# Kernel tuning notes

Hardware: AMD Instinct MI355X
Metric: run time of the kernel (lower is better)

Reference implementation:

```python
import jax, jax.numpy as jnp
import numpy as np

MATRIC_TYPE = 0   # 0: corr, 1: cov
WEIGHT_IN = 1.0
WEIGHT_BET = 1.0


def setup_inputs() -> dict:
    key = jax.random.key(0)
    k1, k2, k3 = jax.random.split(key, 3)
    x = jax.random.normal(k1, (256, 128, 768), dtype=jnp.float32)
    label = jax.random.randint(k2, (256,), 0, 1000, dtype=jnp.int64 if jax.config.read('jax_enable_x64') else jnp.int32)
    genre_label = jax.random.randint(k3, (256,), 0, 8, dtype=jnp.int64 if jax.config.read('jax_enable_x64') else jnp.int32)
    return {"x": x, "label": label, "genre_label": genre_label}


def _compute_various(x):
    # x: [B, N, D] -> within (D,D), between (D,D)
    B, N, D = x.shape
    tol_num = B * N
    x_mean = jnp.mean(x, axis=1)                       # (B, D)
    mean = jnp.mean(x.reshape(-1, D), axis=0)          # (D,)
    res_x = x - x_mean[:, None, :]                     # (B, N, D)
    # fused batched scatter accumulation (replaces python loop of small mms)
    within = jnp.einsum('bnd,bne->de', res_x, res_x) / tol_num
    res_mean = x_mean - mean                           # (B, D)
    between = (N * (res_mean.T @ res_mean)) / tol_num
    return within, between


def _corr_normalize(m):
    # torch code: Diag=(d,1); mm(Diag.T, Diag)=(1,1) scalar = sum(diag^2)
    d = jnp.diagonal(m)
    s = jnp.sqrt(jnp.sum(d * d))
    return m / s


def reference(x, label, genre_label):
    input_x = x[::2]
    input_u = x[1::2]
    x1_within, x1_between = _compute_various(input_x)
    x2_within, x2_between = _compute_various(input_u)
    if MATRIC_TYPE == 0:
        x1_within = _corr_normalize(x1_within)
        x2_within = _corr_normalize(x2_within)
        x1_between = _corr_normalize(x1_between)
        x2_between = _corr_normalize(x2_between)
    within = jnp.sum((x1_within - x2_within) ** 2)
    between = jnp.sum((x1_between - x2_between) ** 2)
    return WEIGHT_IN * within + WEIGHT_BET * between
```

## Files before the change

kernel.cpp:

```cpp
#include <hip/hip_runtime.h>


typedef float f32x2 __attribute__((ext_vector_type(2)));
typedef float f32x4 __attribute__((ext_vector_type(4)));
typedef short bf16x8 __attribute__((ext_vector_type(8)));
typedef unsigned short u16x4 __attribute__((ext_vector_type(4)));

static constexpr size_t OFF_RT    = 0;
static constexpr size_t OFF_XM    = 50331648;
static constexpr size_t OFF_M     = 51118080;
static constexpr size_t OFF_RM    = 51124224;
static constexpr size_t OFF_P2    = 51517440;
static constexpr size_t OFF_BPART = 54269952;
static constexpr size_t OFF_P1    = 54355968;

__device__ __forceinline__ unsigned int f2bf_u32(float f) {
  union { float f; unsigned int u; } v; v.f = f;
  unsigned int u = v.u;
  unsigned int lsb = (u >> 16) & 1u;
  u += 0x7fffu + lsb;
  return u >> 16;
}

__device__ __forceinline__ void gload_lds16(const void* g, void* l) {
  __builtin_amdgcn_global_load_lds(
      (const __attribute__((address_space(1))) unsigned int*)g,
      (__attribute__((address_space(3))) unsigned int*)l, 16, 0, 0);
}

__global__ void __launch_bounds__(256) k1_means_convert(const float* __restrict__ x,
                                                        float* __restrict__ xm,
                                                        unsigned short* __restrict__ RT) {
  __shared__ unsigned short T[128][130];
  __shared__ float pm[4][128];
  int bid = blockIdx.x;
  int dt = bid % 6, borig = bid / 6;
  int s = borig & 1, b = borig >> 1;
  int tid = threadIdx.x, w = tid >> 6, lane = tid & 63;

  const float* xb = x + (size_t)borig * (128 * 768) + dt * 128 + 2 * lane;
  float cs0 = 0.f, cs1 = 0.f;
#pragma unroll
  for (int g = 0; g < 8; ++g) {
    int n0 = w * 32 + g * 4;
    f32x2 a0 = *reinterpret_cast<const f32x2*>(xb + (size_t)(n0 + 0) * 768);
    f32x2 a1 = *reinterpret_cast<const f32x2*>(xb + (size_t)(n0 + 1) * 768);
    f32x2 a2 = *reinterpret_cast<const f32x2*>(xb + (size_t)(n0 + 2) * 768);
    f32x2 a3 = *reinterpret_cast<const f32x2*>(xb + (size_t)(n0 + 3) * 768);
    cs0 += a0[0] + a1[0] + a2[0] + a3[0];
    cs1 += a0[1] + a1[1] + a2[1] + a3[1];
    u16x4 p0, p1;
    p0[0] = (unsigned short)f2bf_u32(a0[0]); p0[1] = (unsigned short)f2bf_u32(a1[0]);
    p0[2] = (unsigned short)f2bf_u32(a2[0]); p0[3] = (unsigned short)f2bf_u32(a3[0]);
    p1[0] = (unsigned short)f2bf_u32(a0[1]); p1[1] = (unsigned short)f2bf_u32(a1[1]);
    p1[2] = (unsigned short)f2bf_u32(a2[1]); p1[3] = (unsigned short)f2bf_u32(a3[1]);
    *reinterpret_cast<u16x4*>(&T[2 * lane + 0][n0]) = p0;
    *reinterpret_cast<u16x4*>(&T[2 * lane + 1][n0]) = p1;
  }
  *reinterpret_cast<f32x2*>(&pm[w][2 * lane]) = f32x2{cs0, cs1};
  __syncthreads();

  if (tid < 128) {
    float mv = (pm[0][tid] + pm[1][tid] + pm[2][tid] + pm[3][tid]) * (1.f / 128.f);
    xm[((size_t)(s * 128 + b)) * 768ull + dt * 128 + tid] = mv;
  }

  int half = lane >> 5;
  int nb = (lane & 31) * 4;
  unsigned short* rtbase = RT + (size_t)s * (768ull * 16384ull) + (size_t)(b * 128 + nb);
#pragma unroll
  for (int i = 0; i < 16; ++i) {
    int d_loc = w * 32 + 2 * i + half;
    uint2 v = *reinterpret_cast<const uint2*>(&T[d_loc][nb]);
    *reinterpret_cast<uint2*>(rtbase + (size_t)(dt * 128 + d_loc) * 16384ull) = v;
  }
}

__global__ void __launch_bounds__(256) k2_slice_mean(const float* __restrict__ xm,
                                                     float* __restrict__ m,
                                                     unsigned short* __restrict__ rmT) {
  __shared__ float pm[4][64];
  __shared__ float ml[64];
  int s = blockIdx.x / 12, dg = blockIdx.x % 12;
  int t = threadIdx.x;
  int d_loc = t & 63, part = t >> 6;
  int d = dg * 64 + d_loc;
  const float* base = xm + (size_t)s * 128ull * 768ull + d;
  float acc = 0.f;
#pragma unroll 4
  for (int i = 0; i < 32; ++i) acc += base[(size_t)(part * 32 + i) * 768ull];
  pm[part][d_loc] = acc;
  __syncthreads();
  if (t < 64) {
    float mv = (pm[0][t] + pm[1][t] + pm[2][t] + pm[3][t]) * (1.f / 128.f);
    m[s * 768 + dg * 64 + t] = mv;
    ml[t] = mv;
  }
  __syncthreads();
  float mv = ml[d_loc];
  unsigned short* rt = rmT + ((size_t)s * 768ull + d) * 128ull + part * 32;
#pragma unroll 4
  for (int i = 0; i < 32; ++i)
    rt[i] = (unsigned short)f2bf_u32(base[(size_t)(part * 32 + i) * 768ull] - mv);
}

__device__ __forceinline__ void stage_tile(const unsigned short* __restrict__ g, int KP, int k0,
                                           unsigned short* lds, int wave, int lane) {
#pragma unroll
  for (int i = 0; i < 4; ++i) {
    int cb = (i * 4 + wave) * 64;
    int chunk = cb + lane;
    int r = chunk >> 3, sl = chunk & 7;
    int ss = sl ^ (r & 7);
    const unsigned short* src = g + (size_t)r * KP + (k0 + ss * 8);
    gload_lds16(src, lds + (size_t)cb * 8);
  }
}

__device__ __forceinline__ bf16x8 read_frag(const unsigned short* lds, int row, int slot) {
  int chunk = row * 8 + (slot ^ (row & 7));
  return *reinterpret_cast<const bf16x8*>(lds + chunk * 8);
}

__device__ __forceinline__ void tp2tile(int tp, int& td, int& te) {
  td = 0; int t2 = tp;
  while (t2 >= 6 - td) { t2 -= 6 - td; ++td; }
  te = td + t2;
}

__global__ void __launch_bounds__(256) gemm_ata(const unsigned short* __restrict__ Rbig,
                                                const unsigned short* __restrict__ rmT,
                                                float* __restrict__ P1, float* __restrict__ P2,
                                                int ksplit) {
  __shared__ unsigned short Ta[2][128 * 64];
  __shared__ unsigned short Tb[2][128 * 64];
  int bid = blockIdx.x;
  const unsigned short* R; size_t slice_stride; int KP;
  int rest, step0, step1; float* pout;
  if (bid < 42 * ksplit) {
    R = Rbig; slice_stride = 768ull * 16384ull; KP = 16384;
    int c = bid % ksplit; rest = bid / ksplit;
    step0 = (256 * c) / ksplit; step1 = (256 * (c + 1)) / ksplit;
    pout = P1 + (size_t)bid * (128 * 128);
  } else {
    int b2 = bid - 42 * ksplit;
    R = rmT; slice_stride = 768ull * 128ull; KP = 128;
    rest = b2; step0 = 0; step1 = 2;
    pout = P2 + (size_t)b2 * (128 * 128);
  }
  int s = rest & 1; int tp = rest >> 1;
  int td, te; tp2tile(tp, td, te);
  bool diag = (td == te);
  const unsigned short* Ra = R + (size_t)s * slice_stride + (size_t)(td * 128) * KP;
  const unsigned short* Rb = R + (size_t)s * slice_stride + (size_t)(te * 128) * KP;
  int tid = threadIdx.x, wave = tid >> 6, lane = tid & 63;
  int m_off = (wave >> 1) * 64, n_off = (wave & 1) * 64;
  int row_a = m_off + (lane & 15), row_b = n_off + (lane & 15);
  f32x4 acc[4][4];
#pragma unroll
  for (int i = 0; i < 4; ++i)
#pragma unroll
    for (int j = 0; j < 4; ++j) { acc[i][j][0]=0.f; acc[i][j][1]=0.f; acc[i][j][2]=0.f; acc[i][j][3]=0.f; }

  stage_tile(Ra, KP, step0 * 64, Ta[0], wave, lane);
  if (!diag) stage_tile(Rb, KP, step0 * 64, Tb[0], wave, lane);
  __syncthreads();

  int cur = 0;
  for (int kt = step0; kt < step1; ++kt) {
    if (kt + 1 < step1) {
      stage_tile(Ra, KP, (kt + 1) * 64, Ta[cur ^ 1], wave, lane);
      if (!diag) stage_tile(Rb, KP, (kt + 1) * 64, Tb[cur ^ 1], wave, lane);
    }
    const unsigned short* Bsrc = diag ? Ta[cur] : Tb[cur];
#pragma unroll
    for (int ks = 0; ks < 2; ++ks) {
      bf16x8 a[4], b[4];
      int slot = ks * 4 + (lane >> 4);
#pragma unroll
      for (int mi = 0; mi < 4; ++mi) a[mi] = read_frag(Ta[cur], row_a + mi * 16, slot);
#pragma unroll
      for (int ni = 0; ni < 4; ++ni) b[ni] = read_frag(Bsrc, row_b + ni * 16, slot);
#pragma unroll
      for (int mi = 0; mi < 4; ++mi)
#pragma unroll
        for (int ni = 0; ni < 4; ++ni)
          acc[mi][ni] = __builtin_amdgcn_mfma_f32_16x16x32_bf16(a[mi], b[ni], acc[mi][ni], 0, 0, 0);
    }
    __syncthreads();
    cur ^= 1;
  }
  int hi = lane >> 4, lo = lane & 15;
#pragma unroll
  for (int mi = 0; mi < 4; ++mi)
#pragma unroll
    for (int ni = 0; ni < 4; ++ni)
#pragma unroll
      for (int r = 0; r < 4; ++r) {
        int rr = m_off + mi * 16 + hi * 4 + r;
        int cc = n_off + ni * 16 + lo;
        pout[rr * 128 + cc] = acc[mi][ni][r];
      }
}

__global__ void __launch_bounds__(256) k5_elem(const float* __restrict__ P1,
                                               const float* __restrict__ P2,
                                               const float* __restrict__ m,
                                               float* __restrict__ bpart, int ksplit) {
  __shared__ float red[4][10];
  int bid = blockIdx.x;
  int tp = bid >> 6;
  int td, te; tp2tile(tp, td, te);
  int idx = ((bid & 63) << 8) + threadIdx.x;
  int r = idx >> 7, cc = idx & 127;
  int d = td * 128 + r, e = te * 128 + cc;
  float W[2], B[2];
  for (int s = 0; s < 2; ++s) {
    const float* base1 = P1 + (size_t)((tp * 2 + s) * ksplit) * 16384ull + idx;
    float g1 = 0.f;
    for (int c6 = 0; c6 < ksplit; ++c6) g1 += base1[(size_t)c6 * 16384ull];
    float p2v = P2[(size_t)(tp * 2 + s) * 16384ull + idx];
    W[s] = g1 - 128.0f * p2v - 16384.0f * m[s * 768 + d] * m[s * 768 + e];
    B[s] = p2v;
  }
  float mult = (td != te) ? 2.0f : 1.0f;
  bool isdiag = (td == te) && (r == cc);
  float v[10];
  v[0] = W[0] * W[0] * mult;  v[1] = W[1] * W[1] * mult;  v[2] = W[0] * W[1] * mult;
  v[3] = B[0] * B[0] * mult;  v[4] = B[1] * B[1] * mult;  v[5] = B[0] * B[1] * mult;
  v[6] = isdiag ? W[0] * W[0] : 0.f;
  v[7] = isdiag ? W[1] * W[1] : 0.f;
  v[8] = isdiag ? B[0] * B[0] : 0.f;
  v[9] = isdiag ? B[1] * B[1] : 0.f;
  int lane = threadIdx.x & 63, w = threadIdx.x >> 6;
#pragma unroll
  for (int off = 32; off; off >>= 1)
#pragma unroll
    for (int j = 0; j < 10; ++j) v[j] += __shfl_down(v[j], off, 64);
  if (lane == 0)
#pragma unroll
    for (int j = 0; j < 10; ++j) red[w][j] = v[j];
  __syncthreads();
  if (threadIdx.x < 10) {
    int j = threadIdx.x;
    bpart[bid * 16 + j] = red[0][j] + red[1][j] + red[2][j] + red[3][j];
  }
}

__global__ void __launch_bounds__(256) k6_final(const float* __restrict__ bpart,
                                                float* __restrict__ out) {
  __shared__ float red[4][10];
  float acc[10];
#pragma unroll
  for (int j = 0; j < 10; ++j) acc[j] = 0.f;
  for (int i = threadIdx.x; i < 1344; i += 256)
#pragma unroll
    for (int j = 0; j < 10; ++j) acc[j] += bpart[i * 16 + j];
  int lane = threadIdx.x & 63, w = threadIdx.x >> 6;
#pragma unroll
  for (int off = 32; off; off >>= 1)
#pragma unroll
    for (int j = 0; j < 10; ++j) acc[j] += __shfl_down(acc[j], off, 64);
  if (lane == 0)
#pragma unroll
    for (int j = 0; j < 10; ++j) red[w][j] = acc[j];
  __syncthreads();
  if (threadIdx.x == 0) {
    float S[10];
#pragma unroll
    for (int j = 0; j < 10; ++j) S[j] = red[0][j] + red[1][j] + red[2][j] + red[3][j];
    float lw = S[0] / S[6] + S[1] / S[7] - 2.0f * S[2] / sqrtf(S[6] * S[7]);
    float lb = S[3] / S[8] + S[4] / S[9] - 2.0f * S[5] / sqrtf(S[8] * S[9]);
    out[0] = lw + lb;
  }
}

extern "C" void kernel_launch(void* const* d_in, const int* in_sizes, int n_in,
                              void* d_out, int out_size, void* d_ws, size_t ws_size,
                              hipStream_t stream) {
  const float* x = (const float*)d_in[0];
  char* ws = (char*)d_ws;
  unsigned short* RT  = (unsigned short*)(ws + OFF_RT);
  float* xm           = (float*)(ws + OFF_XM);
  float* m            = (float*)(ws + OFF_M);
  unsigned short* rmT = (unsigned short*)(ws + OFF_RM);
  float* P2           = (float*)(ws + OFF_P2);
  float* bpart        = (float*)(ws + OFF_BPART);
  float* P1           = (float*)(ws + OFF_P1);
  float* out          = (float*)d_out;

  size_t availP1 = (ws_size > OFF_P1) ? (ws_size - OFF_P1) : 0;
  int ksplit = (int)(availP1 / (42ull * 128 * 128 * 4));
  if (ksplit > 12) ksplit = 12;
  if (ksplit < 1) ksplit = 1;

  hipLaunchKernelGGL(k1_means_convert, dim3(1536), dim3(256), 0, stream, x, xm, RT);
  hipLaunchKernelGGL(k2_slice_mean, dim3(24), dim3(256), 0, stream, xm, m, rmT);
  hipLaunchKernelGGL(gemm_ata, dim3(42 * ksplit + 42), dim3(256), 0, stream,
                     RT, rmT, P1, P2, ksplit);
  hipLaunchKernelGGL(k5_elem, dim3(1344), dim3(256), 0, stream, P1, P2, m, bpart, ksplit);
  hipLaunchKernelGGL(k6_final, dim3(1), dim3(256), 0, stream, bpart, out);
}
```

Baseline: 77.75 us.

## Fuse final reduction into elementwise kernel via last-block atomic counter

Merges the elementwise partial-reduction kernel and the single-block final kernel into one launch. The last block to finish, detected with an atomic counter that the slice-mean kernel resets, performs the final reduction. Each block now handles eight chunks per thread, so the grid shrinks from 1344 to 168 blocks. The split-K cap drops from 12 to 11, giving 504 GEMM blocks instead of 546 and one fewer partial for the elementwise pass to sum. This removes one launch and the tail of a single-block kernel, but the smaller grid may underfill the GPU for a memory-bound pass.

```diff
diff --git a/kernel.cpp b/kernel.cpp
--- a/kernel.cpp
+++ b/kernel.cpp
@@ -12,6 +12,7 @@
 static constexpr size_t OFF_RM    = 51124224;
 static constexpr size_t OFF_P2    = 51517440;
 static constexpr size_t OFF_BPART = 54269952;
+static constexpr size_t OFF_CNT   = 54282240;
 static constexpr size_t OFF_P1    = 54355968;
 
 __device__ __forceinline__ unsigned int f2bf_u32(float f) {
@@ -78,7 +79,9 @@
 
 __global__ void __launch_bounds__(256) k2_slice_mean(const float* __restrict__ xm,
                                                      float* __restrict__ m,
-                                                     unsigned short* __restrict__ rmT) {
+                                                     unsigned short* __restrict__ rmT,
+                                                     unsigned int* __restrict__ cnt) {
+  if (blockIdx.x == 0 && threadIdx.x == 0) cnt[0] = 0u;
   __shared__ float pm[4][64];
   __shared__ float ml[64];
   int s = blockIdx.x / 12, dg = blockIdx.x % 12;
@@ -203,36 +206,46 @@
       }
 }
 
-__global__ void __launch_bounds__(256) k5_elem(const float* __restrict__ P1,
-                                               const float* __restrict__ P2,
-                                               const float* __restrict__ m,
-                                               float* __restrict__ bpart, int ksplit) {
+__global__ void __launch_bounds__(256) k5_fused(const float* __restrict__ P1,
+                                                const float* __restrict__ P2,
+                                                const float* __restrict__ m,
+                                                float* __restrict__ bpart,
+                                                unsigned int* __restrict__ cnt,
+                                                float* __restrict__ out, int ksplit) {
   __shared__ float red[4][10];
+  __shared__ int lastFlag;
   int bid = blockIdx.x;
-  int tp = bid >> 6;
+  int tp = bid >> 3, sub = bid & 7;
   int td, te; tp2tile(tp, td, te);
-  int idx = ((bid & 63) << 8) + threadIdx.x;
-  int r = idx >> 7, cc = idx & 127;
-  int d = td * 128 + r, e = te * 128 + cc;
-  float W[2], B[2];
-  for (int s = 0; s < 2; ++s) {
-    const float* base1 = P1 + (size_t)((tp * 2 + s) * ksplit) * 16384ull + idx;
-    float g1 = 0.f;
-    for (int c6 = 0; c6 < ksplit; ++c6) g1 += base1[(size_t)c6 * 16384ull];
-    float p2v = P2[(size_t)(tp * 2 + s) * 16384ull + idx];
-    W[s] = g1 - 128.0f * p2v - 16384.0f * m[s * 768 + d] * m[s * 768 + e];
-    B[s] = p2v;
-  }
-  float mult = (td != te) ? 2.0f : 1.0f;
-  bool isdiag = (td == te) && (r == cc);
+  bool diagTile = (td == te);
+  float mult = diagTile ? 1.0f : 2.0f;
+  int t = threadIdx.x;
+  int lane = t & 63, w = t >> 6;
   float v[10];
-  v[0] = W[0] * W[0] * mult;  v[1] = W[1] * W[1] * mult;  v[2] = W[0] * W[1] * mult;
-  v[3] = B[0] * B[0] * mult;  v[4] = B[1] * B[1] * mult;  v[5] = B[0] * B[1] * mult;
-  v[6] = isdiag ? W[0] * W[0] : 0.f;
-  v[7] = isdiag ? W[1] * W[1] : 0.f;
-  v[8] = isdiag ? B[0] * B[0] : 0.f;
-  v[9] = isdiag ? B[1] * B[1] : 0.f;
-  int lane = threadIdx.x & 63, w = threadIdx.x >> 6;
+#pragma unroll
+  for (int j = 0; j < 10; ++j) v[j] = 0.f;
+
+  for (int k = 0; k < 8; ++k) {
+    int idx = sub * 2048 + k * 256 + t;
+    int r = idx >> 7, cc = idx & 127;
+    int d = td * 128 + r, e = te * 128 + cc;
+    float W[2], B[2];
+#pragma unroll
+    for (int s = 0; s < 2; ++s) {
+      const float* base1 = P1 + (size_t)((tp * 2 + s) * ksplit) * 16384ull + idx;
+      float g1 = 0.f;
+      for (int c6 = 0; c6 < ksplit; ++c6) g1 += base1[(size_t)c6 * 16384ull];
+      float p2v = P2[(size_t)(tp * 2 + s) * 16384ull + idx];
+      W[s] = g1 - 128.0f * p2v - 16384.0f * m[s * 768 + d] * m[s * 768 + e];
+      B[s] = p2v;
+    }
+    v[0] += W[0] * W[0] * mult;  v[1] += W[1] * W[1] * mult;  v[2] += W[0] * W[1] * mult;
+    v[3] += B[0] * B[0] * mult;  v[4] += B[1] * B[1] * mult;  v[5] += B[0] * B[1] * mult;
+    if (diagTile && r == cc) {
+      v[6] += W[0] * W[0];  v[7] += W[1] * W[1];
+      v[8] += B[0] * B[0];  v[9] += B[1] * B[1];
+    }
+  }
 #pragma unroll
   for (int off = 32; off; off >>= 1)
 #pragma unroll
@@ -241,37 +254,39 @@
 #pragma unroll
     for (int j = 0; j < 10; ++j) red[w][j] = v[j];
   __syncthreads();
-  if (threadIdx.x < 10) {
-    int j = threadIdx.x;
-    bpart[bid * 16 + j] = red[0][j] + red[1][j] + red[2][j] + red[3][j];
-  }
-}
-
-__global__ void __launch_bounds__(256) k6_final(const float* __restrict__ bpart,
-                                                float* __restrict__ out) {
-  __shared__ float red[4][10];
-  float acc[10];
-#pragma unroll
-  for (int j = 0; j < 10; ++j) acc[j] = 0.f;
-  for (int i = threadIdx.x; i < 1344; i += 256)
-#pragma unroll
-    for (int j = 0; j < 10; ++j) acc[j] += bpart[i * 16 + j];
-  int lane = threadIdx.x & 63, w = threadIdx.x >> 6;
-#pragma unroll
-  for (int off = 32; off; off >>= 1)
-#pragma unroll
-    for (int j = 0; j < 10; ++j) acc[j] += __shfl_down(acc[j], off, 64);
-  if (lane == 0)
-#pragma unroll
-    for (int j = 0; j < 10; ++j) red[w][j] = acc[j];
-  __syncthreads();
-  if (threadIdx.x == 0) {
-    float S[10];
-#pragma unroll
-    for (int j = 0; j < 10; ++j) S[j] = red[0][j] + red[1][j] + red[2][j] + red[3][j];
-    float lw = S[0] / S[6] + S[1] / S[7] - 2.0f * S[2] / sqrtf(S[6] * S[7]);
-    float lb = S[3] / S[8] + S[4] / S[9] - 2.0f * S[5] / sqrtf(S[8] * S[9]);
-    out[0] = lw + lb;
+  if (t < 10) bpart[bid * 16 + t] = red[0][t] + red[1][t] + red[2][t] + red[3][t];
+  __threadfence();
+  __syncthreads();
+  if (t == 0) {
+    unsigned int old = atomicAdd(cnt, 1u);
+    lastFlag = (old == 167u) ? 1 : 0;
+  }
+  __syncthreads();
+  if (lastFlag) {
+    __threadfence();
+    float acc[10];
+#pragma unroll
+    for (int j = 0; j < 10; ++j) acc[j] = 0.f;
+    for (int i = t; i < 168; i += 256)
+#pragma unroll
+      for (int j = 0; j < 10; ++j) acc[j] += bpart[i * 16 + j];
+#pragma unroll
+    for (int off = 32; off; off >>= 1)
+#pragma unroll
+      for (int j = 0; j < 10; ++j) acc[j] += __shfl_down(acc[j], off, 64);
+    __syncthreads();
+    if (lane == 0)
+#pragma unroll
+      for (int j = 0; j < 10; ++j) red[w][j] = acc[j];
+    __syncthreads();
+    if (t == 0) {
+      float S[10];
+#pragma unroll
+      for (int j = 0; j < 10; ++j) S[j] = red[0][j] + red[1][j] + red[2][j] + red[3][j];
+      float lw = S[0] / S[6] + S[1] / S[7] - 2.0f * S[2] / sqrtf(S[6] * S[7]);
+      float lb = S[3] / S[8] + S[4] / S[9] - 2.0f * S[5] / sqrtf(S[8] * S[9]);
+      out[0] = lw + lb;
+    }
   }
 }
 
@@ -286,18 +301,19 @@
   unsigned short* rmT = (unsigned short*)(ws + OFF_RM);
   float* P2           = (float*)(ws + OFF_P2);
   float* bpart        = (float*)(ws + OFF_BPART);
+  unsigned int* cnt   = (unsigned int*)(ws + OFF_CNT);
   float* P1           = (float*)(ws + OFF_P1);
   float* out          = (float*)d_out;
 
   size_t availP1 = (ws_size > OFF_P1) ? (ws_size - OFF_P1) : 0;
   int ksplit = (int)(availP1 / (42ull * 128 * 128 * 4));
-  if (ksplit > 12) ksplit = 12;
+  if (ksplit > 11) ksplit = 11;
   if (ksplit < 1) ksplit = 1;
 
   hipLaunchKernelGGL(k1_means_convert, dim3(1536), dim3(256), 0, stream, x, xm, RT);
-  hipLaunchKernelGGL(k2_slice_mean, dim3(24), dim3(256), 0, stream, xm, m, rmT);
+  hipLaunchKernelGGL(k2_slice_mean, dim3(24), dim3(256), 0, stream, xm, m, rmT, cnt);
   hipLaunchKernelGGL(gemm_ata, dim3(42 * ksplit + 42), dim3(256), 0, stream,
                      RT, rmT, P1, P2, ksplit);
-  hipLaunchKernelGGL(k5_elem, dim3(1344), dim3(256), 0, stream, P1, P2, m, bpart, ksplit);
-  hipLaunchKernelGGL(k6_final, dim3(1), dim3(256), 0, stream, bpart, out);
-}
+  hipLaunchKernelGGL(k5_fused, dim3(168), dim3(256), 0, stream,
+                     P1, P2, m, bpart, cnt, out, ksplit);
+}
```

After: 127.3 us. +63.7%, slower.
